# Kernel optimization log

Measured on AMD Instinct MI355X. Metric: run time of the kernel, lower is better.

Reference implementation:

```python
import jax, jax.numpy as jnp
import numpy as np

B, S, E, H, D = 2, 2048, 512, 8, 64
NEG = -1e10


def setup_inputs() -> dict:
    key = jax.random.key(0)
    k1, k2, k3, k4, k5, k6 = jax.random.split(key, 6)
    inputs = jax.random.normal(k1, (B, S, E), dtype=jnp.float32)
    keys = jax.random.normal(k2, (B, S, H, D), dtype=jnp.float32)
    values = jax.random.normal(k3, (B, S, H, D), dtype=jnp.float32)
    # xavier-uniform style scale for square weights
    lim = float(np.sqrt(6.0 / (E + H * D)))
    query_weights = jax.random.uniform(k4, (E, H * D), minval=-lim, maxval=lim, dtype=jnp.float32)
    output_weights = jax.random.uniform(k5, (H * D, E), minval=-lim, maxval=lim, dtype=jnp.float32)
    mask = jax.random.randint(k6, (B, S, S), 0, 2).astype(jnp.bool_)
    return {"inputs": inputs, "keys": keys, "values": values,
            "query_weights": query_weights, "output_weights": output_weights,
            "mask": mask}


def reference(inputs, keys, values, query_weights, output_weights, mask):
    # project queries: (B,S,E) @ (E,H*D) -> (B,S,H,D)
    q = jnp.matmul(inputs, query_weights).reshape(B, S, H, D)
    # scores: (B,H,Sq,Sk)
    scores = jnp.einsum('bqhd,bkhd->bhqk', q, keys) / jnp.sqrt(jnp.float32(D))
    # masked_fill(mask, -1e10); mask broadcasts over heads
    scores = jnp.where(mask[:, None, :, :], jnp.float32(NEG), scores)
    probs = jax.nn.softmax(scores, axis=-1)
    # (B,H,Sq,Sk) x (B,Sk,H,D) -> (B,Sq,H,D)
    out = jnp.einsum('bhqk,bkhd->bqhd', probs, values)
    out = out.reshape(B, S, H * D)
    return jnp.matmul(out, output_weights)
```

## Files before the change

### kernel.cpp

```cpp
#include <hip/hip_runtime.h>
#include <hip/hip_bf16.h>

namespace {

constexpr int B = 2, S = 2048, E = 512, H = 8, D = 64, HD = 512;
constexpr float SL = 0.125f * 1.44269504f;
constexpr int PLD = 40;

typedef __attribute__((ext_vector_type(8))) short bf16x8;
typedef __attribute__((ext_vector_type(4))) unsigned short u16x4;
typedef __attribute__((ext_vector_type(4))) float f32x4;
typedef __attribute__((ext_vector_type(4))) float float4v;

__device__ __forceinline__ ushort f2b(float x) {
  __hip_bfloat16 h = __float2bfloat16(x);
  return *reinterpret_cast<const ushort*>(&h);
}

__global__ __launch_bounds__(256) void prep_fused_kernel(
    const float* __restrict__ K, const float* __restrict__ V,
    const float* __restrict__ Wq, const float* __restrict__ Wo,
    const int* __restrict__ maskp,
    ushort* __restrict__ Kbf, ushort* __restrict__ Vtbf,
    ushort* __restrict__ Wtq, ushort* __restrict__ Wto,
    uint4* __restrict__ keep4) {
  const int bid = blockIdx.x;
  const int t = threadIdx.x;
  if (bid < 512) {
    __shared__ __align__(16) ushort Vn[64][76];
    const int kt = bid & 31;
    const int bh = bid >> 5;
    const int b = bh >> 3, h = bh & 7;
    const int k0 = kt * 64;
#pragma unroll
    for (int i = 0; i < 4; ++i) {
      int c = i * 256 + t;
      int kk = c >> 4, d4 = (c & 15) * 4;
      size_t g = ((size_t)(b * 2048 + k0 + kk) * 8 + h) * 64 + d4;
      float4v kv = *(const float4v*)(K + g);
      float4v vv = *(const float4v*)(V + g);
      u16x4 kp = {f2b(kv.x), f2b(kv.y), f2b(kv.z), f2b(kv.w)};
      u16x4 vp = {f2b(vv.x), f2b(vv.y), f2b(vv.z), f2b(vv.w)};
      *(u16x4*)(Kbf + ((size_t)(bh * 2048 + k0 + kk)) * 64 + d4) = kp;
      *(u16x4*)&Vn[kk][d4] = vp;
    }
    __syncthreads();
#pragma unroll
    for (int i = 0; i < 2; ++i) {
      int c = i * 256 + t;
      int kc8 = (c & 7) * 8, d = c >> 3;
      union { ushort u[8]; bf16x8 v; } p;
#pragma unroll
      for (int j = 0; j < 8; ++j) p.u[j] = Vn[kc8 + j][d];
      *(bf16x8*)(Vtbf + ((size_t)(bh * 64 + d)) * 2048 + k0 + kc8) = p.v;
    }
  } else if (bid < 640) {
    __shared__ __align__(16) ushort T[64][68];
    const int idx = bid - 512;
    const float* Wsrc = (idx >> 6) ? Wo : Wq;
    ushort* Wdst = (idx >> 6) ? Wto : Wtq;
    const int x = idx & 63;
    const int k0 = (x & 7) * 64, n0 = (x >> 3) * 64;
#pragma unroll
    for (int i = 0; i < 4; ++i) {
      int c = i * 256 + t;
      int kk = c >> 4, n4 = (c & 15) * 4;
      float4v v = *(const float4v*)(Wsrc + (size_t)(k0 + kk) * 512 + n0 + n4);
      u16x4 p = {f2b(v.x), f2b(v.y), f2b(v.z), f2b(v.w)};
      *(u16x4*)&T[kk][n4] = p;
    }
    __syncthreads();
#pragma unroll
    for (int i = 0; i < 2; ++i) {
      int c = i * 256 + t;
      int n = c >> 3, k8 = (c & 7) * 8;
      union { ushort u[8]; bf16x8 v; } p;
#pragma unroll
      for (int j = 0; j < 8; ++j) p.u[j] = T[k8 + j][n];
      *(bf16x8*)(Wdst + (size_t)(n0 + n) * 512 + k0 + k8) = p.v;
    }
  } else {
    const int wid = (bid - 640) * 4 + (t >> 6);
    const int row = wid >> 3, c = wid & 7;
    const int lane = t & 63;
    const int4 v = *((const int4*)(maskp + (size_t)row * 2048 + c * 256) + lane);
    unsigned long long bx = __ballot(v.x == 0);
    unsigned long long by = __ballot(v.y == 0);
    unsigned long long bz = __ballot(v.z == 0);
    unsigned long long bw = __ballot(v.w == 0);
    if (lane == 0)
      keep4[(size_t)row * 16 + c * 2] = uint4{(uint)bx, (uint)by, (uint)bz, (uint)bw};
    if (lane == 32)
      keep4[(size_t)row * 16 + c * 2 + 1] =
          uint4{(uint)(bx >> 32), (uint)(by >> 32), (uint)(bz >> 32), (uint)(bw >> 32)};
  }
}

__global__ __launch_bounds__(256) void proj_out_kernel(
    const ushort* __restrict__ A, const ushort* __restrict__ Wt, float* __restrict__ C) {
  __shared__ __align__(16) ushort As[64][PLD];
  __shared__ __align__(16) ushort Ws[64][PLD];

  const int tid = threadIdx.x;
  const int lane = tid & 63;
  const int w = tid >> 6;
  const int col = lane & 15;
  const int quad = lane >> 4;
  const int m0 = blockIdx.y * 64;
  const int n0 = blockIdx.x * 64;
  const int wm = (w & 1) * 32;
  const int wn = (w >> 1) * 32;
  const int ar = tid >> 2;
  const int ak = (tid & 3) * 8;
  const int wn2 = tid >> 2;
  const int wkc = (tid & 3) * 8;

  f32x4 acc[2][2];
#pragma unroll
  for (int i = 0; i < 2; ++i)
#pragma unroll
    for (int j = 0; j < 2; ++j) acc[i][j] = f32x4{0.f, 0.f, 0.f, 0.f};

  const ushort* Ap = A + (size_t)(m0 + ar) * 512 + ak;
  const ushort* Wp = Wt + (size_t)(n0 + wn2) * 512 + wkc;
  bf16x8 apre = *(const bf16x8*)Ap;
  bf16x8 wp = *(const bf16x8*)Wp;

  for (int kt = 0; kt < 16; ++kt) {
    if (kt) __syncthreads();
    *(bf16x8*)&As[ar][ak] = apre;
    *(bf16x8*)&Ws[wn2][wkc] = wp;
    if (kt < 15) {
      const int k1 = (kt + 1) * 32;
      apre = *(const bf16x8*)(Ap + k1);
      wp = *(const bf16x8*)(Wp + k1);
    }
    __syncthreads();

    bf16x8 ah[2], wb[2];
#pragma unroll
    for (int i = 0; i < 2; ++i)
      ah[i] = *(const bf16x8*)&As[wm + i * 16 + col][quad * 8];
#pragma unroll
    for (int j = 0; j < 2; ++j)
      wb[j] = *(const bf16x8*)&Ws[wn + j * 16 + col][quad * 8];
#pragma unroll
    for (int i = 0; i < 2; ++i)
#pragma unroll
      for (int j = 0; j < 2; ++j)
        acc[i][j] = __builtin_amdgcn_mfma_f32_16x16x32_bf16(ah[i], wb[j], acc[i][j], 0, 0, 0);
  }

#pragma unroll
  for (int i = 0; i < 2; ++i)
#pragma unroll
    for (int j = 0; j < 2; ++j)
#pragma unroll
      for (int r = 0; r < 4; ++r)
        C[(size_t)(m0 + wm + i * 16 + (quad << 2) + r) * 512 + n0 + wn + j * 16 + col] =
            acc[i][j][r];
}

__global__ __launch_bounds__(256, 2) void flash_attn_kernel(
    const float* __restrict__ inp, const ushort* __restrict__ Wtq,
    const ushort* __restrict__ Kbf, const ushort* __restrict__ Vtbf,
    const uint4* __restrict__ keep4, ushort* __restrict__ Op) {
  __shared__ __align__(16) union SM {
    struct { ushort Ks[128][72]; ushort Vt[64][136]; ushort PQ[64][72]; } m;
    struct { float red[3][64][68]; float lred[3][64]; } r;
  } sm;

  const int bid = blockIdx.x;
  const int qt = bid & 31;
  const int bh = bid >> 5;
  const int b = bh >> 3, h = bh & 7;
  const int q0 = qt * 64;
  const int tid = threadIdx.x, lane = tid & 63, w = tid >> 6;
  const int col = lane & 15, quad = lane >> 4, quad4 = quad * 4;
  const int wm = (w & 1) * 32;
  const int wn = (w >> 1) * 32;

  {
    const int ar = tid >> 2;
    const int ak = (tid & 3) * 8;

    f32x4 qacc[2][2];
#pragma unroll
    for (int i = 0; i < 2; ++i)
#pragma unroll
      for (int j = 0; j < 2; ++j) qacc[i][j] = f32x4{0.f, 0.f, 0.f, 0.f};

    const float* Ap = inp + (size_t)(b * 2048 + q0 + ar) * 512 + ak;
    const ushort* Wp = Wtq + (size_t)(h * 64 + ar) * 512 + ak;
    float4v a0p = *(const float4v*)Ap;
    float4v a1p = *(const float4v*)(Ap + 4);
    bf16x8 wp = *(const bf16x8*)Wp;

    for (int kt = 0; kt < 16; ++kt) {
      if (kt) __syncthreads();
      {
        union { ushort u[8]; bf16x8 v; } ap;
        ap.u[0] = f2b(a0p.x); ap.u[1] = f2b(a0p.y); ap.u[2] = f2b(a0p.z); ap.u[3] = f2b(a0p.w);
        ap.u[4] = f2b(a1p.x); ap.u[5] = f2b(a1p.y); ap.u[6] = f2b(a1p.z); ap.u[7] = f2b(a1p.w);
        *(bf16x8*)&sm.m.PQ[ar][ak] = ap.v;
        *(bf16x8*)&sm.m.PQ[ar][40 + ak] = wp;
      }
      if (kt < 15) {
        const int k1 = (kt + 1) * 32;
        a0p = *(const float4v*)(Ap + k1);
        a1p = *(const float4v*)(Ap + k1 + 4);
        wp = *(const bf16x8*)(Wp + k1);
      }
      __syncthreads();

      bf16x8 ah[2], wb[2];
#pragma unroll
      for (int i = 0; i < 2; ++i)
        ah[i] = *(const bf16x8*)&sm.m.PQ[wm + i * 16 + col][quad * 8];
#pragma unroll
      for (int j = 0; j < 2; ++j)
        wb[j] = *(const bf16x8*)&sm.m.PQ[wn + j * 16 + col][40 + quad * 8];
#pragma unroll
      for (int i = 0; i < 2; ++i)
#pragma unroll
        for (int j = 0; j < 2; ++j)
          qacc[i][j] = __builtin_amdgcn_mfma_f32_16x16x32_bf16(ah[i], wb[j], qacc[i][j], 0, 0, 0);
    }

    __syncthreads();
#pragma unroll
    for (int i = 0; i < 2; ++i)
#pragma unroll
      for (int j = 0; j < 2; ++j)
#pragma unroll
        for (int r = 0; r < 4; ++r)
          sm.m.PQ[wm + i * 16 + quad4 + r][wn + j * 16 + col] = f2b(qacc[i][j][r]);
    __syncthreads();
  }

  bf16x8 qb[4][2];
#pragma unroll
  for (int j = 0; j < 4; ++j)
#pragma unroll
    for (int hf = 0; hf < 2; ++hf)
      qb[j][hf] = *(const bf16x8*)&sm.m.PQ[j * 16 + col][hf * 32 + quad * 8];

  f32x4 oacc[4][4];
#pragma unroll
  for (int j = 0; j < 4; ++j)
#pragma unroll
    for (int c = 0; c < 4; ++c) oacc[j][c] = f32x4{0.f, 0.f, 0.f, 0.f};
  f32x4 lacc[4];
#pragma unroll
  for (int j = 0; j < 4; ++j) lacc[j] = f32x4{0.f, 0.f, 0.f, 0.f};

  union { ushort u[8]; bf16x8 v; } onesu;
#pragma unroll
  for (int j = 0; j < 8; ++j) onesu.u[j] = 0x3F80;
  const bf16x8 onesB = onesu.v;

  const uint4* kr0 = keep4 + (size_t)(b * 2048 + q0 + col) * 16;
  const ushort* Kbase = Kbf + (size_t)bh * 2048 * 64;
  const ushort* Vbase = Vtbf + (size_t)bh * 64 * 2048;
  const int mshift = 8 * w + quad;

  bf16x8 kpre[4], vpre[4];
#pragma unroll
  for (int i = 0; i < 4; ++i) {
    int c = i * 256 + tid;
    kpre[i] = *(const bf16x8*)(Kbase + (size_t)c * 8);
    int d = c >> 4, k8 = (c & 15) * 8;
    vpre[i] = *(const bf16x8*)(Vbase + (size_t)d * 2048 + k8);
  }

  for (int kt = 0; kt < 16; ++kt) {
    if (kt) __syncthreads();
#pragma unroll
    for (int i = 0; i < 4; ++i) {
      int c = i * 256 + tid;
      *(bf16x8*)&sm.m.Ks[c >> 3][(c & 7) * 8] = kpre[i];
      int d = c >> 4, k8 = (c & 15) * 8;
      *(bf16x8*)&sm.m.Vt[d][k8] = vpre[i];
    }
    uint4 kwj[4];
#pragma unroll
    for (int j = 0; j < 4; ++j) kwj[j] = kr0[j * 256 + kt];
    if (kt < 15) {
      const int k1 = (kt + 1) * 128;
#pragma unroll
      for (int i = 0; i < 4; ++i) {
        int c = i * 256 + tid;
        kpre[i] = *(const bf16x8*)(Kbase + (size_t)k1 * 64 + c * 8);
        int d = c >> 4, k8 = (c & 15) * 8;
        vpre[i] = *(const bf16x8*)(Vbase + (size_t)d * 2048 + k1 + k8);
      }
    }
    __syncthreads();

    bf16x8 ka[2][2];
#pragma unroll
    for (int t = 0; t < 2; ++t)
#pragma unroll
      for (int hf = 0; hf < 2; ++hf)
        ka[t][hf] = *(const bf16x8*)&sm.m.Ks[w * 32 + t * 16 + col][hf * 32 + quad * 8];

    f32x4 sc[2][4];
#pragma unroll
    for (int t = 0; t < 2; ++t)
#pragma unroll
      for (int j = 0; j < 4; ++j) sc[t][j] = f32x4{0.f, 0.f, 0.f, 0.f};
#pragma unroll
    for (int t = 0; t < 2; ++t)
#pragma unroll
      for (int hf = 0; hf < 2; ++hf)
#pragma unroll
        for (int j = 0; j < 4; ++j)
          sc[t][j] = __builtin_amdgcn_mfma_f32_16x16x32_bf16(ka[t][hf], qb[j][hf], sc[t][j], 0, 0, 0);

    bf16x8 vb[4];
#pragma unroll
    for (int c = 0; c < 4; ++c)
      vb[c] = *(const bf16x8*)&sm.m.Vt[c * 16 + col][w * 32 + quad * 8];

#pragma unroll
    for (int j = 0; j < 4; ++j) {
      const uint mx_ = kwj[j].x >> mshift, my_ = kwj[j].y >> mshift,
                 mz_ = kwj[j].z >> mshift, mw_ = kwj[j].w >> mshift;
      uint Xa0, Xa1, Xb0, Xb1;
      {
        float p0 = (mx_ & 1u) ? exp2f(sc[0][j][0] * SL) : 0.f;
        float p1 = (my_ & 1u) ? exp2f(sc[0][j][1] * SL) : 0.f;
        float p2 = (mz_ & 1u) ? exp2f(sc[0][j][2] * SL) : 0.f;
        float p3 = (mw_ & 1u) ? exp2f(sc[0][j][3] * SL) : 0.f;
        __hip_bfloat162 lo = __float22bfloat162_rn(float2{p0, p1});
        __hip_bfloat162 hi = __float22bfloat162_rn(float2{p2, p3});
        Xa0 = *reinterpret_cast<uint*>(&lo);
        Xa1 = *reinterpret_cast<uint*>(&hi);
      }
      {
        float p0 = ((mx_ >> 4) & 1u) ? exp2f(sc[1][j][0] * SL) : 0.f;
        float p1 = ((my_ >> 4) & 1u) ? exp2f(sc[1][j][1] * SL) : 0.f;
        float p2 = ((mz_ >> 4) & 1u) ? exp2f(sc[1][j][2] * SL) : 0.f;
        float p3 = ((mw_ >> 4) & 1u) ? exp2f(sc[1][j][3] * SL) : 0.f;
        __hip_bfloat162 lo = __float22bfloat162_rn(float2{p0, p1});
        __hip_bfloat162 hi = __float22bfloat162_rn(float2{p2, p3});
        Xb0 = *reinterpret_cast<uint*>(&lo);
        Xb1 = *reinterpret_cast<uint*>(&hi);
      }
      auto a32 = __builtin_amdgcn_permlane32_swap(Xa0, Xb0, false, false);
      auto a16 = __builtin_amdgcn_permlane16_swap(a32[0], a32[1], false, false);
      auto b32 = __builtin_amdgcn_permlane32_swap(Xa1, Xb1, false, false);
      auto b16 = __builtin_amdgcn_permlane16_swap(b32[0], b32[1], false, false);
      union { uint u[4]; bf16x8 v; } pu;
      pu.u[0] = a16[0]; pu.u[1] = b16[0]; pu.u[2] = a16[1]; pu.u[3] = b16[1];
      const bf16x8 pa = pu.v;
      lacc[j] = __builtin_amdgcn_mfma_f32_16x16x32_bf16(pa, onesB, lacc[j], 0, 0, 0);
#pragma unroll
      for (int c = 0; c < 4; ++c)
        oacc[j][c] = __builtin_amdgcn_mfma_f32_16x16x32_bf16(pa, vb[c], oacc[j][c], 0, 0, 0);
    }
  }

  __syncthreads();
  if (w > 0) {
    const int wi = w - 1;
#pragma unroll
    for (int j = 0; j < 4; ++j)
#pragma unroll
      for (int c = 0; c < 4; ++c)
        *(f32x4*)&sm.r.red[wi][c * 16 + col][j * 16 + quad4] = oacc[j][c];
    if (col == 0)
#pragma unroll
      for (int j = 0; j < 4; ++j)
        *(f32x4*)&sm.r.lred[wi][j * 16 + quad4] = lacc[j];
  }
  __syncthreads();
  if (w == 0) {
#pragma unroll
    for (int j = 0; j < 4; ++j) {
#pragma unroll
      for (int c = 0; c < 4; ++c) {
        f32x4 s = oacc[j][c];
#pragma unroll
        for (int i = 0; i < 3; ++i)
          s += *(const f32x4*)&sm.r.red[i][c * 16 + col][j * 16 + quad4];
        oacc[j][c] = s;
      }
      f32x4 ls = lacc[j];
#pragma unroll
      for (int i = 0; i < 3; ++i)
        ls += *(const f32x4*)&sm.r.lred[i][j * 16 + quad4];
      lacc[j] = ls;
    }
#pragma unroll
    for (int j = 0; j < 4; ++j) {
#pragma unroll
      for (int c = 0; c < 4; ++c)
        *(f32x4*)&sm.r.red[0][c * 16 + col][j * 16 + quad4] = oacc[j][c];
      if (col == 0) *(f32x4*)&sm.r.lred[0][j * 16 + quad4] = lacc[j];
    }
  }
  __syncthreads();

  {
    const int q = tid >> 2, d0 = (tid & 3) * 16;
    const float inv = 1.f / sm.r.lred[0][q];
    union { ushort u[16]; bf16x8 v[2]; } ob;
#pragma unroll
    for (int dd = 0; dd < 16; ++dd)
      ob.u[dd] = f2b(sm.r.red[0][d0 + dd][q] * inv);
    ushort* dst = Op + (size_t)(b * S + q0 + q) * HD + h * D + d0;
    *(bf16x8*)dst = ob.v[0];
    *(bf16x8*)(dst + 8) = ob.v[1];
  }
}

}

extern "C" void kernel_launch(void* const* d_in, const int* in_sizes, int n_in,
                              void* d_out, int out_size, void* d_ws, size_t ws_size,
                              hipStream_t stream) {
  const float* inputs = (const float*)d_in[0];
  const float* keys   = (const float*)d_in[1];
  const float* values = (const float*)d_in[2];
  const float* wq     = (const float*)d_in[3];
  const float* wo     = (const float*)d_in[4];
  const int*   maskp  = (const int*)d_in[5];
  float* out = (float*)d_out;

  ushort* Kbf  = (ushort*)d_out;
  ushort* Vtbf = Kbf + (size_t)2097152;

  char* ws = (char*)d_ws;
  ushort* attnb = (ushort*)ws;
  uint4*  keep4 = (uint4*)(ws + (4 << 20));
  ushort* Wtq   = (ushort*)(ws + (5 << 20));
  ushort* Wto   = (ushort*)(ws + (5 << 20) + (512 << 10));

  prep_fused_kernel<<<dim3(8832), dim3(256), 0, stream>>>(keys, values, wq, wo, maskp,
                                                          Kbf, Vtbf, Wtq, Wto, keep4);
  flash_attn_kernel<<<dim3(512), dim3(256), 0, stream>>>(inputs, Wtq, Kbf, Vtbf, keep4, attnb);
  proj_out_kernel<<<dim3(8, 64), dim3(256), 0, stream>>>(attnb, Wto, out);
}
```

Baseline: 161.0 us.

## Compute Q projection per-wave from global memory, fold softmax scale, add setprio

The fused Q projection no longer stages input and weight tiles through shared memory with barriers. Each wave now computes its own 16 query rows directly from global loads, covering all 64 head dimensions. The softmax scale is folded into Q before it is converted to bf16, which removes one multiply per score in the exp loop. s_setprio hints are also placed around the MFMA blocks to favour matrix issue across waves. In exchange, each wave reloads the weight rows with no cross-wave reuse, and the pre-scaled Q changes bf16 rounding slightly.

```diff
diff --git a/kernel.cpp b/kernel.cpp
--- a/kernel.cpp
+++ b/kernel.cpp
@@ -166,7 +166,8 @@
     const ushort* __restrict__ Kbf, const ushort* __restrict__ Vtbf,
     const uint4* __restrict__ keep4, ushort* __restrict__ Op) {
   __shared__ __align__(16) union SM {
-    struct { ushort Ks[128][72]; ushort Vt[64][136]; ushort PQ[64][72]; } m;
+    struct { ushort Ks[128][72]; ushort Vt[64][136]; } m;
+    ushort PQ[64][72];
     struct { float red[3][64][68]; float lred[3][64]; } r;
   } sm;
 
@@ -177,73 +178,41 @@
   const int q0 = qt * 64;
   const int tid = threadIdx.x, lane = tid & 63, w = tid >> 6;
   const int col = lane & 15, quad = lane >> 4, quad4 = quad * 4;
-  const int wm = (w & 1) * 32;
-  const int wn = (w >> 1) * 32;
 
   {
-    const int ar = tid >> 2;
-    const int ak = (tid & 3) * 8;
-
-    f32x4 qacc[2][2];
-#pragma unroll
-    for (int i = 0; i < 2; ++i)
-#pragma unroll
-      for (int j = 0; j < 2; ++j) qacc[i][j] = f32x4{0.f, 0.f, 0.f, 0.f};
-
-    const float* Ap = inp + (size_t)(b * 2048 + q0 + ar) * 512 + ak;
-    const ushort* Wp = Wtq + (size_t)(h * 64 + ar) * 512 + ak;
-    float4v a0p = *(const float4v*)Ap;
-    float4v a1p = *(const float4v*)(Ap + 4);
-    bf16x8 wp = *(const bf16x8*)Wp;
-
-    for (int kt = 0; kt < 16; ++kt) {
-      if (kt) __syncthreads();
-      {
-        union { ushort u[8]; bf16x8 v; } ap;
-        ap.u[0] = f2b(a0p.x); ap.u[1] = f2b(a0p.y); ap.u[2] = f2b(a0p.z); ap.u[3] = f2b(a0p.w);
-        ap.u[4] = f2b(a1p.x); ap.u[5] = f2b(a1p.y); ap.u[6] = f2b(a1p.z); ap.u[7] = f2b(a1p.w);
-        *(bf16x8*)&sm.m.PQ[ar][ak] = ap.v;
-        *(bf16x8*)&sm.m.PQ[ar][40 + ak] = wp;
+    f32x4 qacc[4];
+#pragma unroll
+    for (int n = 0; n < 4; ++n) qacc[n] = f32x4{0.f, 0.f, 0.f, 0.f};
+    const float* Ap = inp + (size_t)(b * 2048 + q0 + w * 16 + col) * 512 + quad * 8;
+    const ushort* Wp = Wtq + (size_t)(h * 64 + col) * 512 + quad * 8;
+#pragma unroll 2
+    for (int kk = 0; kk < 16; ++kk) {
+      float4v a0 = *(const float4v*)(Ap + kk * 32);
+      float4v a1 = *(const float4v*)(Ap + kk * 32 + 4);
+      union { ushort u[8]; bf16x8 v; } ap;
+      ap.u[0] = f2b(a0.x); ap.u[1] = f2b(a0.y); ap.u[2] = f2b(a0.z); ap.u[3] = f2b(a0.w);
+      ap.u[4] = f2b(a1.x); ap.u[5] = f2b(a1.y); ap.u[6] = f2b(a1.z); ap.u[7] = f2b(a1.w);
+#pragma unroll
+      for (int n = 0; n < 4; ++n) {
+        bf16x8 wb = *(const bf16x8*)(Wp + (size_t)(n * 16) * 512 + kk * 32);
+        qacc[n] = __builtin_amdgcn_mfma_f32_16x16x32_bf16(ap.v, wb, qacc[n], 0, 0, 0);
       }
-      if (kt < 15) {
-        const int k1 = (kt + 1) * 32;
-        a0p = *(const float4v*)(Ap + k1);
-        a1p = *(const float4v*)(Ap + k1 + 4);
-        wp = *(const bf16x8*)(Wp + k1);
-      }
-      __syncthreads();
-
-      bf16x8 ah[2], wb[2];
-#pragma unroll
-      for (int i = 0; i < 2; ++i)
-        ah[i] = *(const bf16x8*)&sm.m.PQ[wm + i * 16 + col][quad * 8];
-#pragma unroll
-      for (int j = 0; j < 2; ++j)
-        wb[j] = *(const bf16x8*)&sm.m.PQ[wn + j * 16 + col][40 + quad * 8];
-#pragma unroll
-      for (int i = 0; i < 2; ++i)
-#pragma unroll
-        for (int j = 0; j < 2; ++j)
-          qacc[i][j] = __builtin_amdgcn_mfma_f32_16x16x32_bf16(ah[i], wb[j], qacc[i][j], 0, 0, 0);
-    }
-
-    __syncthreads();
-#pragma unroll
-    for (int i = 0; i < 2; ++i)
-#pragma unroll
-      for (int j = 0; j < 2; ++j)
-#pragma unroll
-        for (int r = 0; r < 4; ++r)
-          sm.m.PQ[wm + i * 16 + quad4 + r][wn + j * 16 + col] = f2b(qacc[i][j][r]);
-    __syncthreads();
-  }
+    }
+#pragma unroll
+    for (int n = 0; n < 4; ++n)
+#pragma unroll
+      for (int r = 0; r < 4; ++r)
+        sm.PQ[w * 16 + quad4 + r][n * 16 + col] = f2b(qacc[n][r] * SL);
+  }
+  __syncthreads();
 
   bf16x8 qb[4][2];
 #pragma unroll
   for (int j = 0; j < 4; ++j)
 #pragma unroll
     for (int hf = 0; hf < 2; ++hf)
-      qb[j][hf] = *(const bf16x8*)&sm.m.PQ[j * 16 + col][hf * 32 + quad * 8];
+      qb[j][hf] = *(const bf16x8*)&sm.PQ[j * 16 + col][hf * 32 + quad * 8];
+  __syncthreads();
 
   f32x4 oacc[4][4];
 #pragma unroll
@@ -260,8 +229,8 @@
   const bf16x8 onesB = onesu.v;
 
   const uint4* kr0 = keep4 + (size_t)(b * 2048 + q0 + col) * 16;
-  const ushort* Kbase = Kbf + (size_t)bh * 2048 * 64;
-  const ushort* Vbase = Vtbf + (size_t)bh * 64 * 2048;
+  const ushort* Kbase = Kbf + (size_t)bh * 131072;
+  const ushort* Vbase = Vtbf + (size_t)bh * 131072;
   const int mshift = 8 * w + quad;
 
   bf16x8 kpre[4], vpre[4];
@@ -309,6 +278,7 @@
     for (int t = 0; t < 2; ++t)
 #pragma unroll
       for (int j = 0; j < 4; ++j) sc[t][j] = f32x4{0.f, 0.f, 0.f, 0.f};
+    __builtin_amdgcn_s_setprio(1);
 #pragma unroll
     for (int t = 0; t < 2; ++t)
 #pragma unroll
@@ -316,6 +286,7 @@
 #pragma unroll
         for (int j = 0; j < 4; ++j)
           sc[t][j] = __builtin_amdgcn_mfma_f32_16x16x32_bf16(ka[t][hf], qb[j][hf], sc[t][j], 0, 0, 0);
+    __builtin_amdgcn_s_setprio(0);
 
     bf16x8 vb[4];
 #pragma unroll
@@ -328,20 +299,20 @@
                  mz_ = kwj[j].z >> mshift, mw_ = kwj[j].w >> mshift;
       uint Xa0, Xa1, Xb0, Xb1;
       {
-        float p0 = (mx_ & 1u) ? exp2f(sc[0][j][0] * SL) : 0.f;
-        float p1 = (my_ & 1u) ? exp2f(sc[0][j][1] * SL) : 0.f;
-        float p2 = (mz_ & 1u) ? exp2f(sc[0][j][2] * SL) : 0.f;
-        float p3 = (mw_ & 1u) ? exp2f(sc[0][j][3] * SL) : 0.f;
+        float p0 = (mx_ & 1u) ? exp2f(sc[0][j][0]) : 0.f;
+        float p1 = (my_ & 1u) ? exp2f(sc[0][j][1]) : 0.f;
+        float p2 = (mz_ & 1u) ? exp2f(sc[0][j][2]) : 0.f;
+        float p3 = (mw_ & 1u) ? exp2f(sc[0][j][3]) : 0.f;
         __hip_bfloat162 lo = __float22bfloat162_rn(float2{p0, p1});
         __hip_bfloat162 hi = __float22bfloat162_rn(float2{p2, p3});
         Xa0 = *reinterpret_cast<uint*>(&lo);
         Xa1 = *reinterpret_cast<uint*>(&hi);
       }
       {
-        float p0 = ((mx_ >> 4) & 1u) ? exp2f(sc[1][j][0] * SL) : 0.f;
-        float p1 = ((my_ >> 4) & 1u) ? exp2f(sc[1][j][1] * SL) : 0.f;
-        float p2 = ((mz_ >> 4) & 1u) ? exp2f(sc[1][j][2] * SL) : 0.f;
-        float p3 = ((mw_ >> 4) & 1u) ? exp2f(sc[1][j][3] * SL) : 0.f;
+        float p0 = ((mx_ >> 4) & 1u) ? exp2f(sc[1][j][0]) : 0.f;
+        float p1 = ((my_ >> 4) & 1u) ? exp2f(sc[1][j][1]) : 0.f;
+        float p2 = ((mz_ >> 4) & 1u) ? exp2f(sc[1][j][2]) : 0.f;
+        float p3 = ((mw_ >> 4) & 1u) ? exp2f(sc[1][j][3]) : 0.f;
         __hip_bfloat162 lo = __float22bfloat162_rn(float2{p0, p1});
         __hip_bfloat162 hi = __float22bfloat162_rn(float2{p2, p3});
         Xb0 = *reinterpret_cast<uint*>(&lo);
@@ -354,10 +325,12 @@
       union { uint u[4]; bf16x8 v; } pu;
       pu.u[0] = a16[0]; pu.u[1] = b16[0]; pu.u[2] = a16[1]; pu.u[3] = b16[1];
       const bf16x8 pa = pu.v;
+      __builtin_amdgcn_s_setprio(1);
       lacc[j] = __builtin_amdgcn_mfma_f32_16x16x32_bf16(pa, onesB, lacc[j], 0, 0, 0);
 #pragma unroll
       for (int c = 0; c < 4; ++c)
         oacc[j][c] = __builtin_amdgcn_mfma_f32_16x16x32_bf16(pa, vb[c], oacc[j][c], 0, 0, 0);
+      __builtin_amdgcn_s_setprio(0);
     }
   }
 
```

New measurement: 170.2 us. 1.06x slower.
